# Kernel tuning notes

Hardware: AMD Instinct MI355X
Metric: run time of the kernel (lower is better)

Reference implementation:

```python
import jax, jax.numpy as jnp
import numpy as np

EPS = 1e-6
STEPS = 6  # eval_steps == train_steps == 6


def _l2norm(v, axis, eps=1e-12):
    # F.normalize: v / max(||v||, eps)
    return v / jnp.maximum(jnp.linalg.norm(v, axis=axis, keepdims=True), eps)


def _conv1x1(x, w, b=None):
    # x: [B,C,H,W], w: [O,C]
    y = jnp.einsum('bchw,oc->bohw', x, w)
    if b is not None:
        y = y + b[None, :, None, None]
    return y


def _nmf_local_inference(x, bases):
    # x: [B,D,N], bases: [B,D,R]; torch.no_grad loop
    coef = jax.nn.softmax(jnp.einsum('bdn,bdr->bnr', x, bases), axis=-1)  # inv_t = 1

    def step(carry, _):
        bases, coef = carry
        # coef update
        xtb = jnp.einsum('bdn,bdr->bnr', x, bases)
        btb = jnp.einsum('bdr,bds->brs', bases, bases)
        coef = coef * xtb / (jnp.einsum('bnr,brs->bns', coef, btb) + EPS)
        # bases update
        xc = jnp.einsum('bdn,bnr->bdr', x, coef)
        ctc = jnp.einsum('bnr,bns->brs', coef, coef)
        bases = bases * xc / (jnp.einsum('bdr,brs->bds', bases, ctc) + EPS)
        return (bases, coef), None

    (bases, coef), _ = jax.lax.scan(step, (bases, coef), None, length=STEPS)
    return bases, coef


def _nmf_compute_coef(x, bases, coef):
    # differentiable final coef refinement
    xtb = jnp.einsum('bdn,bdr->bnr', x, bases)
    btb = jnp.einsum('bdr,bds->brs', bases, bases)
    return coef * xtb / (jnp.einsum('bnr,brs->bns', coef, btb) + EPS)


def _ham_nmf(h, bases0):
    # h: [B,C,H,W], S=1 -> D=C, N=H*W
    B, C, H, W = h.shape
    x = h.reshape(B, C, H * W)
    sg = jax.lax.stop_gradient
    bases, coef = _nmf_local_inference(sg(x), bases0)
    bases, coef = sg(bases), sg(coef)
    coef = _nmf_compute_coef(x, bases, coef)
    out = jnp.einsum('bdr,bnr->bdn', bases, coef)  # bases @ coef^T
    return out.reshape(B, C, H, W)


def reference(x, bases0, w_lower, b_lower, w_cheese, b_cheese, w_upper,
              coef_shortcut, coef_ham):
    shortcut = x
    # lower bread: 1x1 conv + ReLU (NMF variant)
    h = jax.nn.relu(_conv1x1(x, w_lower, b_lower))
    # hamburger (NMF2D, spatial=True, rand_init bases normalized over D)
    bases = _l2norm(bases0, axis=1)
    h = _ham_nmf(h, bases)
    # cheese: 1x1 conv + ReLU (norm_cfg=None -> conv has bias)
    h = jax.nn.relu(_conv1x1(h, w_cheese, b_cheese))
    # upper bread: 1x1 conv, no bias
    h = _conv1x1(h, w_upper)
    return jax.nn.relu(coef_ham * h + coef_shortcut * shortcut)


def setup_inputs() -> dict:
    key = jax.random.key(0)
    ks = jax.random.split(key, 8)
    B, in_c, Hh, Ww = 8, 512, 64, 64
    C, R = 512, 64
    std = (2.0 / C) ** 0.5  # kaiming-style init from _init_weight (1x1 convs)
    std_up = (2.0 / in_c) ** 0.5
    return {
        'x': jax.random.normal(ks[0], (B, in_c, Hh, Ww), jnp.float32),
        'bases0': jax.random.uniform(ks[1], (B, C, R), jnp.float32),
        'w_lower': jax.random.normal(ks[2], (C, in_c), jnp.float32) * std,
        'b_lower': jnp.zeros((C,), jnp.float32),
        'w_cheese': jax.random.normal(ks[3], (C, C), jnp.float32) * std,
        'b_cheese': jnp.zeros((C,), jnp.float32),
        'w_upper': jax.random.normal(ks[4], (in_c, C), jnp.float32) * std_up,
        'coef_shortcut': jnp.ones((1,), jnp.float32),
        'coef_ham': jnp.ones((1,), jnp.float32),
    }
```

## Files before the change

### kernel.cpp

```cpp
#include <hip/hip_runtime.h>

#define NMF_EPS 1e-6f

typedef unsigned short ushort_t;
typedef __attribute__((ext_vector_type(8))) short bf16x8;
typedef __attribute__((ext_vector_type(4))) float f32x4;

__device__ __forceinline__ ushort_t f2bf(float f) {
    unsigned int u = __float_as_uint(f);
    return (ushort_t)((u + 0x7FFFu + ((u >> 16) & 1u)) >> 16);
}
__device__ __forceinline__ float bf2f(ushort_t h) {
    return __uint_as_float(((unsigned int)h) << 16);
}

__device__ __forceinline__ void gl_lds16(const ushort_t* g, ushort_t* l) {
    __builtin_amdgcn_global_load_lds(
        (const __attribute__((address_space(1))) unsigned int*)g,
        (__attribute__((address_space(3))) unsigned int*)l,
        16, 0, 0);
}

template<int SPLIT, int EPI>
__global__ __launch_bounds__(256) void mfma_gemm(
    const ushort_t* __restrict__ Ah, const ushort_t* __restrict__ Al,
    const ushort_t* __restrict__ Bh, const ushort_t* __restrict__ Bl,
    float* __restrict__ C, ushort_t* __restrict__ Chi, ushort_t* __restrict__ Clo,
    int M, int N, int K,
    long sB, long sC,
    const float* __restrict__ bias,
    const float* __restrict__ res, long sRes,
    const float* __restrict__ hamp, const float* __restrict__ scp)
{
    constexpr int SB = SPLIT ? 32768 : 16384;
    __shared__ char smem[2 * SB];

    const int tid  = threadIdx.x;
    const int wave = tid >> 6, lane = tid & 63;
    const int quad = lane >> 4, lr = lane & 15;
    const int batch = blockIdx.z;
    const int m0 = blockIdx.y * 128, n0 = blockIdx.x * 128;

    const ushort_t* Bhb = Bh + (long)batch * sB;
    const ushort_t* Blb = SPLIT ? (Bl + (long)batch * sB) : nullptr;

    f32x4 acc[4][4];
    #pragma unroll
    for (int i = 0; i < 4; ++i)
        #pragma unroll
        for (int j = 0; j < 4; ++j)
            acc[i][j] = (f32x4){0.f, 0.f, 0.f, 0.f};

    const int q   = wave * 2;
    const int ra0 = (q + 0) * 16 + (lane >> 2);
    const int ra1 = (q + 1) * 16 + (lane >> 2);
    const int ko  = (lane & 3) * 8;
    const int wm = (wave & 1) * 64, wn = (wave >> 1) * 64;

    auto STAGE = [&](int buf, int k0) {
        char* base = smem + buf * SB;
        ushort_t* dAh = (ushort_t*)base;
        ushort_t* dBh = (ushort_t*)(base + 8192);
        gl_lds16(&Ah [(long)(m0 + ra0) * K + k0 + ko], &dAh[(q + 0) * 512]);
        gl_lds16(&Ah [(long)(m0 + ra1) * K + k0 + ko], &dAh[(q + 1) * 512]);
        gl_lds16(&Bhb[(long)(n0 + ra0) * K + k0 + ko], &dBh[(q + 0) * 512]);
        gl_lds16(&Bhb[(long)(n0 + ra1) * K + k0 + ko], &dBh[(q + 1) * 512]);
        if constexpr (SPLIT) {
            ushort_t* dAl = (ushort_t*)(base + 16384);
            ushort_t* dBl = (ushort_t*)(base + 24576);
            gl_lds16(&Al [(long)(m0 + ra0) * K + k0 + ko], &dAl[(q + 0) * 512]);
            gl_lds16(&Al [(long)(m0 + ra1) * K + k0 + ko], &dAl[(q + 1) * 512]);
            gl_lds16(&Blb[(long)(n0 + ra0) * K + k0 + ko], &dBl[(q + 0) * 512]);
            gl_lds16(&Blb[(long)(n0 + ra1) * K + k0 + ko], &dBl[(q + 1) * 512]);
        }
    };

    STAGE(0, 0);
    __syncthreads();
    int cur = 0;

    for (int k0 = 0; k0 < K; k0 += 32) {
        if (k0 + 32 < K) STAGE(cur ^ 1, k0 + 32);

        char* base = smem + cur * SB;
        ushort_t* sAh = (ushort_t*)base;
        ushort_t* sBh = (ushort_t*)(base + 8192);

        bf16x8 af[4], bfr[4], afl[4], bfl[4];
        #pragma unroll
        for (int i = 0; i < 4; ++i)
            af[i] = *(const bf16x8*)&sAh[(wm + i * 16 + lr) * 32 + quad * 8];
        #pragma unroll
        for (int j = 0; j < 4; ++j)
            bfr[j] = *(const bf16x8*)&sBh[(wn + j * 16 + lr) * 32 + quad * 8];
        if constexpr (SPLIT) {
            ushort_t* sAl = (ushort_t*)(base + 16384);
            ushort_t* sBl = (ushort_t*)(base + 24576);
            #pragma unroll
            for (int i = 0; i < 4; ++i)
                afl[i] = *(const bf16x8*)&sAl[(wm + i * 16 + lr) * 32 + quad * 8];
            #pragma unroll
            for (int j = 0; j < 4; ++j)
                bfl[j] = *(const bf16x8*)&sBl[(wn + j * 16 + lr) * 32 + quad * 8];
        }

        #pragma unroll
        for (int i = 0; i < 4; ++i)
            #pragma unroll
            for (int j = 0; j < 4; ++j) {
                acc[i][j] = __builtin_amdgcn_mfma_f32_16x16x32_bf16(af[i], bfr[j], acc[i][j], 0, 0, 0);
                if constexpr (SPLIT) {
                    acc[i][j] = __builtin_amdgcn_mfma_f32_16x16x32_bf16(af[i], bfl[j], acc[i][j], 0, 0, 0);
                    acc[i][j] = __builtin_amdgcn_mfma_f32_16x16x32_bf16(afl[i], bfr[j], acc[i][j], 0, 0, 0);
                }
            }
        __syncthreads();
        cur ^= 1;
    }

    if (EPI == 2) {
        ushort_t* Hh = Chi + (long)batch * sC;
        ushort_t* Hl = Clo + (long)batch * sC;
        unsigned int* slab = (unsigned int*)smem;
        #pragma unroll
        for (int p = 0; p < 2; ++p) {
            __syncthreads();
            if ((wave & 1) == p) {
                #pragma unroll
                for (int i = 0; i < 4; ++i) {
                    const int mb = m0 + p * 64 + i * 16 + quad * 4;
                    #pragma unroll
                    for (int j = 0; j < 4; ++j) {
                        const int nl = wn + j * 16 + lr;
                        #pragma unroll
                        for (int r = 0; r < 4; ++r) {
                            float v = fmaxf(acc[i][j][r] + bias[mb + r], 0.f);
                            ushort_t h = f2bf(v);
                            ushort_t l = f2bf(v - bf2f(h));
                            slab[nl * 64 + (i * 16 + quad * 4 + r)] =
                                (unsigned)h | ((unsigned)l << 16);
                        }
                    }
                }
            }
            __syncthreads();
            for (int idx = tid; idx < 8192; idx += 256) {
                const int nl = idx >> 6, ml = idx & 63;
                unsigned u = slab[idx];
                const long off = (long)(n0 + nl) * M + m0 + p * 64 + ml;
                Hh[off] = (ushort_t)(u & 0xffffu);
                Hl[off] = (ushort_t)(u >> 16);
            }
        }
    } else {
        const float hm = *hamp, sc = *scp;
        float* Cb = C + (long)batch * sC;
        #pragma unroll
        for (int i = 0; i < 4; ++i) {
            #pragma unroll
            for (int j = 0; j < 4; ++j) {
                const int mbase = m0 + wm + i * 16 + quad * 4;
                const int n     = n0 + wn + j * 16 + lr;
                #pragma unroll
                for (int r = 0; r < 4; ++r) {
                    float rv = res[(long)batch * sRes + (long)(mbase + r) * N + n];
                    Cb[(long)(mbase + r) * N + n] = fmaxf(fmaf(hm, acc[i][j][r], sc * rv), 0.f);
                }
            }
        }
    }
}

template<int MODE>
__global__ __launch_bounds__(256) void coef_step(
    const ushort_t* __restrict__ Xh, const ushort_t* __restrict__ Xl,
    const ushort_t* __restrict__ bth, const ushort_t* __restrict__ btl,
    const float* __restrict__ btb_part,
    float* __restrict__ coef,
    ushort_t* __restrict__ cth, ushort_t* __restrict__ ctl,
    float* __restrict__ ctc_part,
    int Bcnt)
{
    constexpr bool MU = (MODE >= 1);
    __shared__ char smem[32768 + 18432];
    ushort_t* stg = (ushort_t*)smem;
    ushort_t* gLh = (ushort_t*)(smem + 32768);
    ushort_t* gLl = gLh + 64 * 72;

    const int tid = threadIdx.x, wave = tid >> 6, lane = tid & 63;
    const int quad = lane >> 4, lr = lane & 15;
    const int b = blockIdx.y, n0 = blockIdx.x * 64;

    const ushort_t* Xhb  = Xh  + (long)b * 2097152 + (long)n0 * 512;
    const ushort_t* Xlb  = Xl  + (long)b * 2097152 + (long)n0 * 512;
    const ushort_t* bthb = bth + (long)b * 32768;
    const ushort_t* btlb = btl + (long)b * 32768;
    float* coefB = coef + (long)b * 262144 + (long)n0 * 64;

    if (MU) {
        for (int i = tid; i < 4096; i += 256) {
            const int r = i >> 6, s = i & 63;
            float v = 0.f;
            #pragma unroll
            for (int c = 0; c < 8; ++c)
                v += btb_part[((long)c * Bcnt + b) * 4096 + i];
            ushort_t h = f2bf(v);
            gLh[r * 72 + s] = h;
            gLl[r * 72 + s] = f2bf(v - bf2f(h));
        }
    }

    const int srow = wave * 16 + (lane >> 2);
    const int koff = (lane & 3) * 8;
    f32x4 accx[4];
    #pragma unroll
    for (int j = 0; j < 4; ++j) accx[j] = (f32x4){0.f, 0.f, 0.f, 0.f};

    auto STAGEX = [&](int buf, int kc) {
        const int kg = kc * 32 + koff;
        gl_lds16(&Xhb [(long)srow * 512 + kg], &stg[buf * 8192 + 0 * 2048 + wave * 512]);
        gl_lds16(&Xlb [(long)srow * 512 + kg], &stg[buf * 8192 + 1 * 2048 + wave * 512]);
        gl_lds16(&bthb[(long)srow * 512 + kg], &stg[buf * 8192 + 2 * 2048 + wave * 512]);
        gl_lds16(&btlb[(long)srow * 512 + kg], &stg[buf * 8192 + 3 * 2048 + wave * 512]);
    };

    STAGEX(0, 0);
    __syncthreads();
    int cur = 0;

    for (int kc = 0; kc < 16; ++kc) {
        if (kc + 1 < 16) STAGEX(cur ^ 1, kc + 1);
        bf16x8 ah = *(const bf16x8*)&stg[cur * 8192 + 0 * 2048 + (wave * 16 + lr) * 32 + quad * 8];
        bf16x8 al = *(const bf16x8*)&stg[cur * 8192 + 1 * 2048 + (wave * 16 + lr) * 32 + quad * 8];
        #pragma unroll
        for (int j = 0; j < 4; ++j) {
            bf16x8 bh = *(const bf16x8*)&stg[cur * 8192 + 2 * 2048 + (j * 16 + lr) * 32 + quad * 8];
            bf16x8 bl = *(const bf16x8*)&stg[cur * 8192 + 3 * 2048 + (j * 16 + lr) * 32 + quad * 8];
            accx[j] = __builtin_amdgcn_mfma_f32_16x16x32_bf16(ah, bh, accx[j], 0, 0, 0);
            accx[j] = __builtin_amdgcn_mfma_f32_16x16x32_bf16(ah, bl, accx[j], 0, 0, 0);
            accx[j] = __builtin_amdgcn_mfma_f32_16x16x32_bf16(al, bh, accx[j], 0, 0, 0);
        }
        __syncthreads();
        cur ^= 1;
    }

    float cnew[4][4];
    if (MU) {
        f32x4 accd[4];
        #pragma unroll
        for (int j = 0; j < 4; ++j) accd[j] = (f32x4){0.f, 0.f, 0.f, 0.f};
        #pragma unroll
        for (int kk = 0; kk < 2; ++kk) {
            const float* cp = &coefB[(wave * 16 + lr) * 64 + kk * 32 + quad * 8];
            float4 cA = *(const float4*)cp;
            float4 cB = *(const float4*)(cp + 4);
            float cv[8] = {cA.x, cA.y, cA.z, cA.w, cB.x, cB.y, cB.z, cB.w};
            bf16x8 ah, al;
            #pragma unroll
            for (int e = 0; e < 8; ++e) {
                ushort_t h = f2bf(cv[e]);
                ((short*)&ah)[e] = (short)h;
                ((short*)&al)[e] = (short)f2bf(cv[e] - bf2f(h));
            }
            #pragma unroll
            for (int j = 0; j < 4; ++j) {
                bf16x8 bh = *(const bf16x8*)&gLh[(j * 16 + lr) * 72 + kk * 32 + quad * 8];
                bf16x8 bl = *(const bf16x8*)&gLl[(j * 16 + lr) * 72 + kk * 32 + quad * 8];
                accd[j] = __builtin_amdgcn_mfma_f32_16x16x32_bf16(ah, bh, accd[j], 0, 0, 0);
                accd[j] = __builtin_amdgcn_mfma_f32_16x16x32_bf16(ah, bl, accd[j], 0, 0, 0);
                accd[j] = __builtin_amdgcn_mfma_f32_16x16x32_bf16(al, bh, accd[j], 0, 0, 0);
            }
        }
        #pragma unroll
        for (int j = 0; j < 4; ++j)
            #pragma unroll
            for (int r = 0; r < 4; ++r) {
                float cold = coefB[(wave * 16 + quad * 4 + r) * 64 + j * 16 + lr];
                cnew[j][r] = cold * accx[j][r] / (accd[j][r] + NMF_EPS);
            }
    } else {
        #pragma unroll
        for (int r = 0; r < 4; ++r) {
            float m = fmaxf(fmaxf(accx[0][r], accx[1][r]), fmaxf(accx[2][r], accx[3][r]));
            #pragma unroll
            for (int off = 1; off < 16; off <<= 1) m = fmaxf(m, __shfl_xor(m, off, 64));
            float e[4], s = 0.f;
            #pragma unroll
            for (int j = 0; j < 4; ++j) { e[j] = __expf(accx[j][r] - m); s += e[j]; }
            #pragma unroll
            for (int off = 1; off < 16; off <<= 1) s += __shfl_xor(s, off, 64);
            float inv = 1.f / s;
            #pragma unroll
            for (int j = 0; j < 4; ++j) cnew[j][r] = e[j] * inv;
        }
    }

    #pragma unroll
    for (int j = 0; j < 4; ++j)
        #pragma unroll
        for (int r = 0; r < 4; ++r)
            coefB[(wave * 16 + quad * 4 + r) * 64 + j * 16 + lr] = cnew[j][r];

    if (MODE != 1) return;

    __syncthreads();
    #pragma unroll
    for (int j = 0; j < 4; ++j)
        #pragma unroll
        for (int r = 0; r < 4; ++r) {
            const int nl = wave * 16 + quad * 4 + r;
            const int rr = j * 16 + lr;
            float v = cnew[j][r];
            ushort_t h = f2bf(v);
            gLh[rr * 72 + nl] = h;
            gLl[rr * 72 + nl] = f2bf(v - bf2f(h));
        }
    __syncthreads();
    for (int i = tid; i < 4096; i += 256) {
        const int r = i >> 6, nn = i & 63;
        cth[(long)b * 262144 + (long)r * 4096 + n0 + nn] = gLh[r * 72 + nn];
        ctl[(long)b * 262144 + (long)r * 4096 + n0 + nn] = gLl[r * 72 + nn];
    }
    f32x4 accc[4];
    #pragma unroll
    for (int j = 0; j < 4; ++j) accc[j] = (f32x4){0.f, 0.f, 0.f, 0.f};
    #pragma unroll
    for (int kk = 0; kk < 64; kk += 32) {
        bf16x8 ah = *(const bf16x8*)&gLh[(wave * 16 + lr) * 72 + kk + quad * 8];
        bf16x8 al = *(const bf16x8*)&gLl[(wave * 16 + lr) * 72 + kk + quad * 8];
        #pragma unroll
        for (int j = 0; j < 4; ++j) {
            bf16x8 bh = *(const bf16x8*)&gLh[(j * 16 + lr) * 72 + kk + quad * 8];
            bf16x8 bl = *(const bf16x8*)&gLl[(j * 16 + lr) * 72 + kk + quad * 8];
            accc[j] = __builtin_amdgcn_mfma_f32_16x16x32_bf16(ah, bh, accc[j], 0, 0, 0);
            accc[j] = __builtin_amdgcn_mfma_f32_16x16x32_bf16(ah, bl, accc[j], 0, 0, 0);
            accc[j] = __builtin_amdgcn_mfma_f32_16x16x32_bf16(al, bh, accc[j], 0, 0, 0);
        }
    }
    float* cp = ctc_part + ((long)blockIdx.x * Bcnt + b) * 4096;
    #pragma unroll
    for (int j = 0; j < 4; ++j)
        #pragma unroll
        for (int r = 0; r < 4; ++r)
            cp[(wave * 16 + quad * 4 + r) * 64 + j * 16 + lr] = accc[j][r];
}

__global__ __launch_bounds__(256) void ctc_reduce(const float* __restrict__ part,
                                                  float* __restrict__ ctc, int Bcnt)
{
    const int b = blockIdx.x >> 4;
    const int i = (blockIdx.x & 15) * 256 + threadIdx.x;
    float v = 0.f;
    #pragma unroll 8
    for (int c = 0; c < 64; ++c)
        v += part[((long)c * Bcnt + b) * 4096 + i];
    ctc[(long)b * 4096 + i] = v;
}

__global__ __launch_bounds__(256) void xc_partial(
    const ushort_t* __restrict__ Ah, const ushort_t* __restrict__ Al,
    const ushort_t* __restrict__ Bh, const ushort_t* __restrict__ Bl,
    float* __restrict__ part, int Bcnt)
{
    __shared__ ushort_t stg[2 * 8192];
    const int tid = threadIdx.x, wave = tid >> 6, lane = tid & 63;
    const int quad = lane >> 4, lr = lane & 15;
    const int batch = blockIdx.z;
    const int m0 = blockIdx.y * 64;
    const int k0 = blockIdx.x * 512;

    const ushort_t* Ab  = Ah + (long)batch * 2097152;
    const ushort_t* Alb = Al + (long)batch * 2097152;
    const ushort_t* Bb  = Bh + (long)batch * 262144;
    const ushort_t* Blb = Bl + (long)batch * 262144;

    const int srow = wave * 16 + (lane >> 2);
    const int koff = (lane & 3) * 8;

    f32x4 acc[4];
    #pragma unroll
    for (int j = 0; j < 4; ++j) acc[j] = (f32x4){0.f, 0.f, 0.f, 0.f};

    auto STAGEX = [&](int buf, int kc) {
        const int kg = k0 + kc * 32 + koff;
        gl_lds16(&Ab [(long)(m0 + srow) * 4096 + kg], &stg[buf * 8192 + 0 * 2048 + wave * 512]);
        gl_lds16(&Alb[(long)(m0 + srow) * 4096 + kg], &stg[buf * 8192 + 1 * 2048 + wave * 512]);
        gl_lds16(&Bb [(long)srow * 4096 + kg], &stg[buf * 8192 + 2 * 2048 + wave * 512]);
        gl_lds16(&Blb[(long)srow * 4096 + kg], &stg[buf * 8192 + 3 * 2048 + wave * 512]);
    };

    STAGEX(0, 0);
    __syncthreads();
    int cur = 0;

    for (int kc = 0; kc < 16; ++kc) {
        if (kc + 1 < 16) STAGEX(cur ^ 1, kc + 1);
        bf16x8 ah = *(const bf16x8*)&stg[cur * 8192 + 0 * 2048 + (wave * 16 + lr) * 32 + quad * 8];
        bf16x8 al = *(const bf16x8*)&stg[cur * 8192 + 1 * 2048 + (wave * 16 + lr) * 32 + quad * 8];
        #pragma unroll
        for (int j = 0; j < 4; ++j) {
            bf16x8 bh = *(const bf16x8*)&stg[cur * 8192 + 2 * 2048 + (j * 16 + lr) * 32 + quad * 8];
            bf16x8 bl = *(const bf16x8*)&stg[cur * 8192 + 3 * 2048 + (j * 16 + lr) * 32 + quad * 8];
            acc[j] = __builtin_amdgcn_mfma_f32_16x16x32_bf16(ah, bh, acc[j], 0, 0, 0);
            acc[j] = __builtin_amdgcn_mfma_f32_16x16x32_bf16(ah, bl, acc[j], 0, 0, 0);
            acc[j] = __builtin_amdgcn_mfma_f32_16x16x32_bf16(al, bh, acc[j], 0, 0, 0);
        }
        __syncthreads();
        cur ^= 1;
    }

    float* Cb = part + ((long)blockIdx.x * Bcnt + batch) * 32768;
    #pragma unroll
    for (int j = 0; j < 4; ++j) {
        const int col = j * 16 + lr;
        #pragma unroll
        for (int r = 0; r < 4; ++r)
            Cb[(long)(m0 + wave * 16 + quad * 4 + r) * 64 + col] = acc[j][r];
    }
}

template<int MODE>
__global__ __launch_bounds__(256) void bases_step(
    const float* __restrict__ xc_part,
    const float* __restrict__ ctc,
    float* __restrict__ bases,
    ushort_t* __restrict__ bth, ushort_t* __restrict__ btl,
    float* __restrict__ btb_part,
    int Bcnt)
{
    __shared__ char smem[16640 * 2 + 18432];
    float* bnL  = (float*)smem;
    float* ctcL = (float*)(smem + 16640);
    ushort_t* btLh = (ushort_t*)(smem + 33280);
    ushort_t* btLl = btLh + 64 * 72;
    float* basesL = (float*)(smem + 33280);

    const int b = blockIdx.y, c0 = blockIdx.x * 64;
    const int tid = threadIdx.x;
    float* basesB = bases + (long)b * 32768 + (long)c0 * 64;

    if (MODE == 1) {
        for (int i = tid; i < 4096; i += 256) {
            const int c = i >> 6, r = i & 63;
            basesL[c * 65 + r] = basesB[i];
            ctcL[c * 65 + r]   = ctc[(long)b * 4096 + i];
            float v = 0.f;
            #pragma unroll
            for (int s0 = 0; s0 < 8; ++s0)
                v += xc_part[((long)s0 * Bcnt + b) * 32768 + (long)(c0 + c) * 64 + r];
            bnL[c * 65 + r] = v;
        }
        __syncthreads();
        for (int i = tid; i < 4096; i += 256) {
            const int c = i >> 6, r = i & 63;
            float denom = 0.f;
            #pragma unroll 8
            for (int s = 0; s < 64; ++s)
                denom = fmaf(basesL[c * 65 + s], ctcL[s * 65 + r], denom);
            float bnew = basesL[c * 65 + r] * bnL[c * 65 + r] / (denom + NMF_EPS);
            bnL[c * 65 + r] = bnew;
            basesB[i] = bnew;
        }
        __syncthreads();
    } else {
        for (int i = tid; i < 4096; i += 256)
            bnL[(i >> 6) * 65 + (i & 63)] = basesB[i];
        __syncthreads();
    }

    for (int i = tid; i < 4096; i += 256) {
        const int r = i >> 6, cc = i & 63;
        float v = bnL[cc * 65 + r];
        ushort_t h = f2bf(v);
        ushort_t l = f2bf(v - bf2f(h));
        btLh[r * 72 + cc] = h;
        btLl[r * 72 + cc] = l;
        bth[(long)b * 32768 + (long)r * 512 + c0 + cc] = h;
        btl[(long)b * 32768 + (long)r * 512 + c0 + cc] = l;
    }
    __syncthreads();

    const int wave = tid >> 6, lane = tid & 63;
    const int quad = lane >> 4, lr = lane & 15;
    f32x4 acg[4];
    #pragma unroll
    for (int j = 0; j < 4; ++j) acg[j] = (f32x4){0.f, 0.f, 0.f, 0.f};
    #pragma unroll
    for (int kk = 0; kk < 64; kk += 32) {
        bf16x8 ah = *(const bf16x8*)&btLh[(wave * 16 + lr) * 72 + kk + quad * 8];
        bf16x8 al = *(const bf16x8*)&btLl[(wave * 16 + lr) * 72 + kk + quad * 8];
        #pragma unroll
        for (int j = 0; j < 4; ++j) {
            bf16x8 bh = *(const bf16x8*)&btLh[(j * 16 + lr) * 72 + kk + quad * 8];
            bf16x8 bl = *(const bf16x8*)&btLl[(j * 16 + lr) * 72 + kk + quad * 8];
            acg[j] = __builtin_amdgcn_mfma_f32_16x16x32_bf16(ah, bh, acg[j], 0, 0, 0);
            acg[j] = __builtin_amdgcn_mfma_f32_16x16x32_bf16(ah, bl, acg[j], 0, 0, 0);
            acg[j] = __builtin_amdgcn_mfma_f32_16x16x32_bf16(al, bh, acg[j], 0, 0, 0);
        }
    }
    float* gp = btb_part + ((long)blockIdx.x * Bcnt + b) * 4096;
    #pragma unroll
    for (int j = 0; j < 4; ++j)
        #pragma unroll
        for (int r = 0; r < 4; ++r)
            gp[(wave * 16 + quad * 4 + r) * 64 + j * 16 + lr] = acg[j][r];
}

constexpr int BM = 64, BN = 64, BK = 16;

template<int ALAY, int BLAY, int EPI>
__global__ __launch_bounds__(256) void gemm_kernel(
    const float* __restrict__ A, const float* __restrict__ B, float* __restrict__ C,
    int Kchunk, int kchunks,
    int lda, int ldb, int ldc,
    long sA, long sB, long sC,
    const float* __restrict__ bias)
{
    __shared__ float As[BK][BM + 4];
    __shared__ float Bs[BK][BN + 4];

    const int batch = blockIdx.z;
    const float* Ab = A + (long)batch * sA;
    const float* Bb = B + (long)batch * sB;

    const int m0  = blockIdx.y * BM;
    const int n0  = blockIdx.x * BN;
    const int tid = threadIdx.x;
    const int ty  = tid >> 4, tx = tid & 15;

    float acc[4][4] = {};

    for (int kt = 0; kt < Kchunk; kt += BK) {
        if (ALAY == 0) {
            const int m = tid >> 2, k4 = (tid & 3) << 2;
            float4 v = *(const float4*)&Ab[(long)(m0 + m) * lda + (kt + k4)];
            As[k4 + 0][m] = v.x; As[k4 + 1][m] = v.y;
            As[k4 + 2][m] = v.z; As[k4 + 3][m] = v.w;
        } else {
            const int k = tid >> 4, m4 = (tid & 15) << 2;
            float4 v = *(const float4*)&Ab[(long)(kt + k) * lda + (m0 + m4)];
            *(float4*)&As[k][m4] = v;
        }
        if (BLAY == 0) {
            const int k = tid >> 4, n4 = (tid & 15) << 2;
            float4 v = *(const float4*)&Bb[(long)(kt + k) * ldb + (n0 + n4)];
            *(float4*)&Bs[k][n4] = v;
        } else {
            const int n = tid >> 2, k4 = (tid & 3) << 2;
            float4 v = *(const float4*)&Bb[(long)(n0 + n) * ldb + (kt + k4)];
            Bs[k4 + 0][n] = v.x; Bs[k4 + 1][n] = v.y;
            Bs[k4 + 2][n] = v.z; Bs[k4 + 3][n] = v.w;
        }
        __syncthreads();
        #pragma unroll
        for (int k = 0; k < BK; ++k) {
            float4 a4 = *(const float4*)&As[k][ty << 2];
            float4 b4 = *(const float4*)&Bs[k][tx << 2];
            float av[4] = {a4.x, a4.y, a4.z, a4.w};
            float bv[4] = {b4.x, b4.y, b4.z, b4.w};
            #pragma unroll
            for (int i = 0; i < 4; ++i)
                #pragma unroll
                for (int j = 0; j < 4; ++j)
                    acc[i][j] = fmaf(av[i], bv[j], acc[i][j]);
        }
        __syncthreads();
    }

    const int mb = m0 + (ty << 2), nb = n0 + (tx << 2);
    if (EPI == 4) {
        ushort_t* Cu = (ushort_t*)C + (long)batch * sC;
        #pragma unroll
        for (int j = 0; j < 4; ++j) {
            ushort_t pk[4];
            #pragma unroll
            for (int i = 0; i < 4; ++i)
                pk[i] = f2bf(fmaxf(acc[i][j] + bias[mb + i], 0.f));
            *(ushort4*)&Cu[(long)(nb + j) * ldc + mb] =
                make_ushort4(pk[0], pk[1], pk[2], pk[3]);
        }
    } else {
        float* Cb = C + (long)batch * sC;
        #pragma unroll
        for (int i = 0; i < 4; ++i) {
            float4 o = make_float4(acc[i][0], acc[i][1], acc[i][2], acc[i][3]);
            *(float4*)&Cb[(long)(mb + i) * ldc + nb] = o;
        }
    }
}

__global__ __launch_bounds__(256) void cast_x_t(const float* __restrict__ x,
                                                ushort_t* __restrict__ hi,
                                                ushort_t* __restrict__ lo)
{
    __shared__ float t[64][65];
    const int b = blockIdx.z, c0 = blockIdx.y * 64, n0 = blockIdx.x * 64;
    const int tid = threadIdx.x, tx = tid & 63, ty = tid >> 6;
    const float* xb = x + (long)b * 512 * 4096;
    #pragma unroll 4
    for (int s = ty; s < 64; s += 4)
        t[s][tx] = xb[(long)(c0 + s) * 4096 + n0 + tx];
    __syncthreads();
    #pragma unroll 4
    for (int s = ty; s < 64; s += 4) {
        float v = t[tx][s];
        long idx = (long)b * 2097152 + (long)(n0 + s) * 512 + c0 + tx;
        ushort_t h = f2bf(v);
        hi[idx] = h;
        lo[idx] = f2bf(v - bf2f(h));
    }
}

__global__ __launch_bounds__(256) void nd2dn(const ushort_t* __restrict__ hi,
                                             const ushort_t* __restrict__ lo,
                                             ushort_t* __restrict__ dhi,
                                             ushort_t* __restrict__ dlo)
{
    __shared__ unsigned int t[64][65];
    const int b = blockIdx.z, n0 = blockIdx.x * 64, c0 = blockIdx.y * 64;
    const int tx = threadIdx.x & 63, ty = threadIdx.x >> 6;
    const long base = (long)b * 2097152;
    #pragma unroll 4
    for (int s = ty; s < 64; s += 4) {
        long idx = base + (long)(n0 + s) * 512 + c0 + tx;
        t[s][tx] = (unsigned)hi[idx] | ((unsigned)lo[idx] << 16);
    }
    __syncthreads();
    #pragma unroll 4
    for (int s = ty; s < 64; s += 4) {
        unsigned v = t[tx][s];
        long idx = base + (long)(c0 + s) * 4096 + n0 + tx;
        dhi[idx] = (ushort_t)(v & 0xffffu);
        dlo[idx] = (ushort_t)(v >> 16);
    }
}

__global__ void cast_w_split(const float* __restrict__ w, ushort_t* __restrict__ hi,
                             ushort_t* __restrict__ lo, int n)
{
    int i = blockIdx.x * 256 + threadIdx.x;
    if (i < n) {
        float v = w[i];
        ushort_t h = f2bf(v);
        hi[i] = h;
        lo[i] = f2bf(v - bf2f(h));
    }
}

__global__ void cast_w_plain(const float* __restrict__ w, ushort_t* __restrict__ o, int n)
{
    int i = blockIdx.x * 256 + threadIdx.x;
    if (i < n) o[i] = f2bf(w[i]);
}

__global__ __launch_bounds__(1024) void l2norm_kernel(const float* __restrict__ b0,
                                                      float* __restrict__ bases)
{
    __shared__ float part[16][64];
    const int b = blockIdx.x;
    const int tid = threadIdx.x;
    const int r = tid & 63, slice = tid >> 6;
    const float* src = b0 + (long)b * 512 * 64;
    float* dst = bases + (long)b * 512 * 64;
    float s = 0.f;
    #pragma unroll 4
    for (int d = slice; d < 512; d += 16) {
        float v = src[d * 64 + r];
        s = fmaf(v, v, s);
    }
    part[slice][r] = s;
    __syncthreads();
    if (slice == 0) {
        float t = 0.f;
        #pragma unroll
        for (int i = 0; i < 16; ++i) t += part[i][r];
        part[0][r] = 1.0f / fmaxf(sqrtf(t), 1e-12f);
    }
    __syncthreads();
    const float inv = part[0][r];
    #pragma unroll 4
    for (int d = slice; d < 512; d += 16)
        dst[d * 64 + r] = src[d * 64 + r] * inv;
}

extern "C" void kernel_launch(void* const* d_in, const int* in_sizes, int n_in,
                              void* d_out, int out_size, void* d_ws, size_t ws_size,
                              hipStream_t stream)
{
    const float* x_in     = (const float*)d_in[0];
    const float* bases0   = (const float*)d_in[1];
    const float* w_lower  = (const float*)d_in[2];
    const float* b_lower  = (const float*)d_in[3];
    const float* w_cheese = (const float*)d_in[4];
    const float* b_cheese = (const float*)d_in[5];
    const float* w_upper  = (const float*)d_in[6];
    const float* csc      = (const float*)d_in[7];
    const float* cham     = (const float*)d_in[8];
    float* out = (float*)d_out;

    const int B = 8, C = 512, N = 4096, R = 64;
    const long sCN = (long)C * N;
    const long sNC = (long)N * C;
    const long sNR = (long)N * R, sCR = (long)C * R;

    char* w = (char*)d_ws;
    ushort_t* X_nd_hi  = (ushort_t*)w;  w += 33554432;
    ushort_t* xt_hi    = (ushort_t*)w;  w += 33554432;
    ushort_t* xt_lo    = (ushort_t*)w;  w += 33554432;
    float*    coef     = (float*)w;     w += 8388608;
    ushort_t* ct_hi    = (ushort_t*)w;  w += 4194304;
    ushort_t* ct_lo    = (ushort_t*)w;  w += 4194304;
    float*    ctc_part = (float*)w;     w += 8388608;
    float*    xc_part  = (float*)w;     w += 8388608;
    float*    btb_part = (float*)w;     w += 1048576;
    float*    bases    = (float*)w;     w += 1048576;
    float*    WcB      = (float*)w;     w += 1048576;
    float*    ctc      = (float*)w;     w += 131072;
    ushort_t* bt_hi    = (ushort_t*)w;  w += 524288;
    ushort_t* bt_lo    = (ushort_t*)w;  w += 524288;
    ushort_t* wl_hi    = (ushort_t*)w;  w += 524288;
    ushort_t* wl_lo    = (ushort_t*)w;  w += 524288;
    ushort_t* w_up     = (ushort_t*)w;  w += 524288;

    ushort_t* X_nd_lo;
    {
        const size_t used = (size_t)(w - (char*)d_ws);
        if (ws_size >= used + 33554432UL) {
            X_nd_lo = (ushort_t*)w;  w += 33554432;
        } else {
            X_nd_lo = (ushort_t*)d_out;
        }
    }

    ushort_t* X_dn_hi  = xt_hi;
    ushort_t* X_dn_lo  = xt_lo;
    ushort_t* cheese_t = X_nd_hi;

    const dim3 blk(256);

    l2norm_kernel<<<dim3(B), dim3(1024), 0, stream>>>(bases0, bases);
    bases_step<0><<<dim3(C / 64, B), blk, 0, stream>>>(
        nullptr, nullptr, bases, bt_hi, bt_lo, btb_part, B);
    cast_w_split<<<dim3(1024), blk, 0, stream>>>(w_lower, wl_hi, wl_lo, C * C);
    cast_w_plain<<<dim3(1024), blk, 0, stream>>>(w_upper, w_up, C * C);
    cast_x_t<<<dim3(N / 64, C / 64, B), blk, 0, stream>>>(x_in, xt_hi, xt_lo);

    mfma_gemm<1, 2><<<dim3(N / 128, C / 128, B), blk, 0, stream>>>(
        wl_hi, wl_lo, xt_hi, xt_lo, nullptr, X_nd_hi, X_nd_lo,
        C, N, C, sNC, sNC, b_lower, nullptr, 0L, nullptr, nullptr);
    nd2dn<<<dim3(N / 64, C / 64, B), blk, 0, stream>>>(X_nd_hi, X_nd_lo, X_dn_hi, X_dn_lo);

    coef_step<0><<<dim3(N / 64, B), blk, 0, stream>>>(
        X_nd_hi, X_nd_lo, bt_hi, bt_lo, btb_part, coef, ct_hi, ct_lo, ctc_part, B);

    for (int step = 0; step < 6; ++step) {
        coef_step<1><<<dim3(N / 64, B), blk, 0, stream>>>(
            X_nd_hi, X_nd_lo, bt_hi, bt_lo, btb_part, coef, ct_hi, ct_lo, ctc_part, B);
        ctc_reduce<<<dim3(B * 16), blk, 0, stream>>>(ctc_part, ctc, B);
        xc_partial<<<dim3(8, C / 64, B), blk, 0, stream>>>(
            X_dn_hi, X_dn_lo, ct_hi, ct_lo, xc_part, B);
        bases_step<1><<<dim3(C / 64, B), blk, 0, stream>>>(
            xc_part, ctc, bases, bt_hi, bt_lo, btb_part, B);
    }

    coef_step<2><<<dim3(N / 64, B), blk, 0, stream>>>(
        X_nd_hi, X_nd_lo, bt_hi, bt_lo, btb_part, coef, ct_hi, ct_lo, ctc_part, B);

    gemm_kernel<0, 0, 0><<<dim3(1, C / BM, B), blk, 0, stream>>>(
        w_cheese, bases, WcB, C, 1, C, R, R, 0L, sCR, sCR, nullptr);
    gemm_kernel<0, 1, 4><<<dim3(N / BN, C / BM, B), blk, 0, stream>>>(
        WcB, coef, (float*)cheese_t, R, 1, R, R, C, sCR, sNR, sNC, b_cheese);

    mfma_gemm<0, 3><<<dim3(N / 128, C / 128, B), blk, 0, stream>>>(
        w_up, nullptr, cheese_t, nullptr, out, nullptr, nullptr,
        C, N, C, sNC, sCN, nullptr, x_in, sCN, cham, csc);
}
```

Baseline: 768.3 us.

## Deepen LDS pipeline to triple buffering with explicit vmcnt waits and raw barriers

In coef_step and xc_partial, async global-to-LDS staging moves from double to triple buffering, keeping two tiles in flight. The mfma_gemm and staging loops swap __syncthreads for explicit s_waitcnt vmcnt plus raw s_barrier and sched_barrier fences. The goal is to hide global load latency that the old full-drain syncs exposed. In exchange it uses more LDS per block, which may lower occupancy, and relies on hand-counted vmcnt values being right.

```diff
diff --git a/kernel.cpp b/kernel.cpp
--- a/kernel.cpp
+++ b/kernel.cpp
@@ -20,6 +20,10 @@
         (__attribute__((address_space(3))) unsigned int*)l,
         16, 0, 0);
 }
+
+#define WAIT_VMCNT(N) asm volatile("s_waitcnt vmcnt(" #N ")" ::: "memory")
+#define SCHED_FENCE() __builtin_amdgcn_sched_barrier(0)
+#define RAW_BAR()     __builtin_amdgcn_s_barrier()
 
 template<int SPLIT, int EPI>
 __global__ __launch_bounds__(256) void mfma_gemm(
@@ -78,9 +82,18 @@
     STAGE(0, 0);
     __syncthreads();
     int cur = 0;
-
-    for (int k0 = 0; k0 < K; k0 += 32) {
-        if (k0 + 32 < K) STAGE(cur ^ 1, k0 + 32);
+    const int NT = K >> 5;
+
+    for (int t = 0; t < NT; ++t) {
+        if (t + 1 < NT) {
+            STAGE(cur ^ 1, (t + 1) << 5);
+            if constexpr (SPLIT) { WAIT_VMCNT(8); } else { WAIT_VMCNT(4); }
+        } else {
+            WAIT_VMCNT(0);
+        }
+        SCHED_FENCE();
+        RAW_BAR();
+        SCHED_FENCE();
 
         char* base = smem + cur * SB;
         ushort_t* sAh = (ushort_t*)base;
@@ -114,7 +127,8 @@
                     acc[i][j] = __builtin_amdgcn_mfma_f32_16x16x32_bf16(afl[i], bfr[j], acc[i][j], 0, 0, 0);
                 }
             }
-        __syncthreads();
+        RAW_BAR();
+        SCHED_FENCE();
         cur ^= 1;
     }
 
@@ -182,9 +196,9 @@
     int Bcnt)
 {
     constexpr bool MU = (MODE >= 1);
-    __shared__ char smem[32768 + 18432];
+    __shared__ char smem[49152 + 18432];
     ushort_t* stg = (ushort_t*)smem;
-    ushort_t* gLh = (ushort_t*)(smem + 32768);
+    ushort_t* gLh = (ushort_t*)(smem + 49152);
     ushort_t* gLl = gLh + 64 * 72;
 
     const int tid = threadIdx.x, wave = tid >> 6, lane = tid & 63;
@@ -225,23 +239,36 @@
     };
 
     STAGEX(0, 0);
-    __syncthreads();
-    int cur = 0;
-
-    for (int kc = 0; kc < 16; ++kc) {
-        if (kc + 1 < 16) STAGEX(cur ^ 1, kc + 1);
-        bf16x8 ah = *(const bf16x8*)&stg[cur * 8192 + 0 * 2048 + (wave * 16 + lr) * 32 + quad * 8];
-        bf16x8 al = *(const bf16x8*)&stg[cur * 8192 + 1 * 2048 + (wave * 16 + lr) * 32 + quad * 8];
+    STAGEX(1, 1);
+    __syncthreads();
+
+    int b0 = 0, b1 = 1, b2 = 2;
+    for (int t = 0; t < 16; ++t) {
+        if (t < 14) {
+            STAGEX(b2, t + 2);
+            WAIT_VMCNT(8);
+        } else if (t == 14) {
+            WAIT_VMCNT(4);
+        } else {
+            WAIT_VMCNT(0);
+        }
+        SCHED_FENCE();
+        RAW_BAR();
+        SCHED_FENCE();
+
+        bf16x8 ah = *(const bf16x8*)&stg[b0 * 8192 + 0 * 2048 + (wave * 16 + lr) * 32 + quad * 8];
+        bf16x8 al = *(const bf16x8*)&stg[b0 * 8192 + 1 * 2048 + (wave * 16 + lr) * 32 + quad * 8];
         #pragma unroll
         for (int j = 0; j < 4; ++j) {
-            bf16x8 bh = *(const bf16x8*)&stg[cur * 8192 + 2 * 2048 + (j * 16 + lr) * 32 + quad * 8];
-            bf16x8 bl = *(const bf16x8*)&stg[cur * 8192 + 3 * 2048 + (j * 16 + lr) * 32 + quad * 8];
+            bf16x8 bh = *(const bf16x8*)&stg[b0 * 8192 + 2 * 2048 + (j * 16 + lr) * 32 + quad * 8];
+            bf16x8 bl = *(const bf16x8*)&stg[b0 * 8192 + 3 * 2048 + (j * 16 + lr) * 32 + quad * 8];
             accx[j] = __builtin_amdgcn_mfma_f32_16x16x32_bf16(ah, bh, accx[j], 0, 0, 0);
             accx[j] = __builtin_amdgcn_mfma_f32_16x16x32_bf16(ah, bl, accx[j], 0, 0, 0);
             accx[j] = __builtin_amdgcn_mfma_f32_16x16x32_bf16(al, bh, accx[j], 0, 0, 0);
         }
-        __syncthreads();
-        cur ^= 1;
+        RAW_BAR();
+        SCHED_FENCE();
+        int tmp = b0; b0 = b1; b1 = b2; b2 = tmp;
     }
 
     float cnew[4][4];
@@ -362,7 +389,7 @@
     const ushort_t* __restrict__ Bh, const ushort_t* __restrict__ Bl,
     float* __restrict__ part, int Bcnt)
 {
-    __shared__ ushort_t stg[2 * 8192];
+    __shared__ ushort_t stg[3 * 8192];
     const int tid = threadIdx.x, wave = tid >> 6, lane = tid & 63;
     const int quad = lane >> 4, lr = lane & 15;
     const int batch = blockIdx.z;
@@ -390,23 +417,36 @@
     };
 
     STAGEX(0, 0);
-    __syncthreads();
-    int cur = 0;
-
-    for (int kc = 0; kc < 16; ++kc) {
-        if (kc + 1 < 16) STAGEX(cur ^ 1, kc + 1);
-        bf16x8 ah = *(const bf16x8*)&stg[cur * 8192 + 0 * 2048 + (wave * 16 + lr) * 32 + quad * 8];
-        bf16x8 al = *(const bf16x8*)&stg[cur * 8192 + 1 * 2048 + (wave * 16 + lr) * 32 + quad * 8];
+    STAGEX(1, 1);
+    __syncthreads();
+
+    int b0 = 0, b1 = 1, b2 = 2;
+    for (int t = 0; t < 16; ++t) {
+        if (t < 14) {
+            STAGEX(b2, t + 2);
+            WAIT_VMCNT(8);
+        } else if (t == 14) {
+            WAIT_VMCNT(4);
+        } else {
+            WAIT_VMCNT(0);
+        }
+        SCHED_FENCE();
+        RAW_BAR();
+        SCHED_FENCE();
+
+        bf16x8 ah = *(const bf16x8*)&stg[b0 * 8192 + 0 * 2048 + (wave * 16 + lr) * 32 + quad * 8];
+        bf16x8 al = *(const bf16x8*)&stg[b0 * 8192 + 1 * 2048 + (wave * 16 + lr) * 32 + quad * 8];
         #pragma unroll
         for (int j = 0; j < 4; ++j) {
-            bf16x8 bh = *(const bf16x8*)&stg[cur * 8192 + 2 * 2048 + (j * 16 + lr) * 32 + quad * 8];
-            bf16x8 bl = *(const bf16x8*)&stg[cur * 8192 + 3 * 2048 + (j * 16 + lr) * 32 + quad * 8];
+            bf16x8 bh = *(const bf16x8*)&stg[b0 * 8192 + 2 * 2048 + (j * 16 + lr) * 32 + quad * 8];
+            bf16x8 bl = *(const bf16x8*)&stg[b0 * 8192 + 3 * 2048 + (j * 16 + lr) * 32 + quad * 8];
             acc[j] = __builtin_amdgcn_mfma_f32_16x16x32_bf16(ah, bh, acc[j], 0, 0, 0);
             acc[j] = __builtin_amdgcn_mfma_f32_16x16x32_bf16(ah, bl, acc[j], 0, 0, 0);
             acc[j] = __builtin_amdgcn_mfma_f32_16x16x32_bf16(al, bh, acc[j], 0, 0, 0);
         }
-        __syncthreads();
-        cur ^= 1;
+        RAW_BAR();
+        SCHED_FENCE();
+        int tmp = b0; b0 = b1; b1 = b2; b2 = tmp;
     }
 
     float* Cb = part + ((long)blockIdx.x * Bcnt + batch) * 32768;
```

After: 757.6 us. About the same (-1.4%).
